# Kernel optimization log

Hardware: AMD Instinct MI355X
Metric: run time of the kernel (lower is better)

The kernel has to match this reference:

```python
import jax, jax.numpy as jnp
import numpy as np

CHANNELS = 32


def _mlp(x, W1, b1, W2, b2, W3, b3):
    # FNN: Linear -> ReLU -> Linear -> ReLU -> Linear (last layer linear)
    h = jax.nn.relu(x @ W1 + b1)
    h = jax.nn.relu(h @ W2 + b2)
    return h @ W3 + b3


def setup_inputs() -> dict:
    key = jax.random.key(0)
    ks = jax.random.split(key, 8)
    E = 262144
    C = CHANNELS
    H = 128
    d_in = 4  # 2 * spatial_dim
    d_out = C * (C + 1)  # 1056
    s = lambda fan_in: 1.0 / np.sqrt(fan_in)
    return {
        "pos_i": jax.random.normal(ks[0], (E, 2), jnp.float32),
        "pos_j": jax.random.normal(ks[1], (E, 2), jnp.float32),
        "v_j": jax.random.normal(ks[2], (E, C), jnp.float32),
        "W1": jax.random.normal(ks[3], (d_in, H), jnp.float32) * s(d_in),
        "b1": jnp.zeros((H,), jnp.float32),
        "W2": jax.random.normal(ks[4], (H, H), jnp.float32) * s(H),
        "b2": jnp.zeros((H,), jnp.float32),
        "W3": jax.random.normal(ks[5], (H, d_out), jnp.float32) * s(H),
        "b3": jnp.zeros((d_out,), jnp.float32),
    }


def reference(pos_i, pos_j, v_j, W1, b1, W2, b2, W3, b3):
    C = CHANNELS
    pos_ij = jnp.concatenate((pos_i, pos_j), axis=-1)          # [E, 2*spatial_dim]
    kernel = _mlp(pos_ij, W1, b1, W2, b2, W3, b3)
    kernel = kernel.reshape(-1, C, C + 1)                      # [E, C, C+1]
    mat, bias = kernel[..., :, :-1], kernel[..., :, -1]        # [E,C,C], [E,C]
    return jnp.einsum('eij,ej->ei', mat, v_j) + bias           # [E, C]
```

## Files before the change

### kernel.cpp

```cpp
#include <hip/hip_runtime.h>


#define E_TOTAL 262144
#define EPB 256
#define NBLK (E_TOTAL / EPB)
#define NEED_WS (524288ull + 67108864ull)

typedef float f32x4 __attribute__((ext_vector_type(4)));
typedef short s8v  __attribute__((ext_vector_type(8)));
typedef unsigned int u32;

__device__ __forceinline__ unsigned short f2bf(float x) {
  unsigned u = __float_as_uint(x);
  u += 0x7fffu + ((u >> 16) & 1u);
  return (unsigned short)(u >> 16);
}

__device__ __forceinline__ void ld16_g2l(const void* g, void* l) {
  __builtin_amdgcn_global_load_lds((const __attribute__((address_space(1))) u32*)g,
                                   (__attribute__((address_space(3))) u32*)l, 16, 0, 0);
}

__global__ void prep_pack(const float* __restrict__ W2, const float* __restrict__ W3,
                          const float* __restrict__ b3,
                          unsigned short* __restrict__ Wg2, unsigned short* __restrict__ W2f,
                          unsigned short* __restrict__ b3f, float* __restrict__ b3c) {
  int idx = blockIdx.x * 256 + threadIdx.x;
  if (idx < 135168) {
    int k = idx / 1056, c = idx % 1056;
    int i = c / 33, jc = c % 33;
    int col = jc * 32 + i;
    int nnt = col >> 4, low = col & 15;
    int nn = (nnt & 1) ? (33 + (nnt >> 1)) : (nnt >> 1);
    int ks = k >> 5, kr = k & 31;
    int lane = ((kr >> 3) << 4) + low;
    int jj = k & 7;
    Wg2[((nn * 4 + ks) * 64 + lane) * 8 + jj] = f2bf(W3[idx]);
  }
  if (idx < 16384) {
    int k = idx >> 7, n = idx & 127;
    int ks = k >> 5, kr = k & 31;
    int nt = n >> 4, low = n & 15;
    int l = ((kr >> 3) << 4) + low;
    int jj = k & 7;
    W2f[((ks * 8 + nt) * 64 + l) * 8 + jj] = f2bf(W2[idx]);
  }
  if (idx < 1024) {
    int jj = idx & 7, lane = (idx >> 3) & 63, ih = idx >> 9;
    int j = ((lane >> 4) << 3) + jj, i = ih * 16 + (lane & 15);
    b3f[idx] = f2bf(b3[i * 33 + j]);
  }
  if (idx < 32) b3c[idx] = b3[idx * 33 + 32];
}

__global__ __launch_bounds__(256, 3) void h2_pass(
    const float* __restrict__ pos_i, const float* __restrict__ pos_j,
    const float* __restrict__ W1, const float* __restrict__ b1,
    const float* __restrict__ b2, const unsigned short* __restrict__ W2f,
    unsigned short* __restrict__ h2frag) {
  __shared__ __attribute__((aligned(16))) char smem[67584];
  unsigned short* h1c = (unsigned short*)smem;
  unsigned short* h2n = (unsigned short*)(smem + 17408);
  unsigned short* W2L = (unsigned short*)(smem + 34816);

  const int tid = threadIdx.x;
  const int w = tid >> 6, lane = tid & 63, q = lane >> 4, ln = lane & 15;
  const int B0 = blockIdx.x * EPB;

  {
    const unsigned short* src = W2f + tid * 8;
    char* dstb = smem + 34816 + w * 1024;
#pragma unroll
    for (int cc = 0; cc < 8; ++cc)
      ld16_g2l(src + cc * 2048, dstb + cc * 4096);
  }

  const int hh0 = (tid & 15) * 8;
  float w1r[4][8], b1r[8], b2r[8];
#pragma unroll
  for (int d = 0; d < 4; ++d)
#pragma unroll
    for (int u = 0; u < 8; ++u) w1r[d][u] = W1[d * 128 + hh0 + u];
#pragma unroll
  for (int u = 0; u < 8; ++u) b1r[u] = b1[hh0 + u];
#pragma unroll
  for (int s = 0; s < 8; ++s) b2r[s] = b2[s * 16 + ln];

  for (int qtr = 0; qtr < 4; ++qtr) {
#pragma unroll
    for (int half = 0; half < 4; ++half) {
      int ee = (tid >> 4) + half * 16;
      int eg = B0 + qtr * 64 + ee;
      float2 pi = *(const float2*)(pos_i + (size_t)eg * 2);
      float2 pj = *(const float2*)(pos_j + (size_t)eg * 2);
      s8v hv;
#pragma unroll
      for (int u = 0; u < 8; ++u) {
        float o = b1r[u] + pi.x * w1r[0][u] + pi.y * w1r[1][u] +
                  pj.x * w1r[2][u] + pj.y * w1r[3][u];
        hv[u] = (short)f2bf(fmaxf(o, 0.f));
      }
      *(s8v*)&h1c[ee * 136 + hh0] = hv;
    }
    __syncthreads();

#pragma unroll
    for (int s = 0; s < 8; ++s) {
      f32x4 a4 = {0.f, 0.f, 0.f, 0.f};
#pragma unroll
      for (int ks = 0; ks < 4; ++ks) {
        s8v afr = *(const s8v*)&h1c[(w * 16 + ln) * 136 + ks * 32 + q * 8];
        s8v bfr = *(const s8v*)&W2L[((ks * 8 + s) * 64 + lane) * 8];
        a4 = __builtin_amdgcn_mfma_f32_16x16x32_bf16(afr, bfr, a4, 0, 0, 0);
      }
      int eb = w * 16 + q * 4;
      int kc = s * 16 + ln;
#pragma unroll
      for (int r = 0; r < 4; ++r)
        h2n[(eb + r) * 136 + kc] = f2bf(fmaxf(a4[r] + b2r[s], 0.f));
    }
    __syncthreads();

    {
      int f = tid >> 4, g = f >> 2, ks = f & 3, s = tid & 15;
      unsigned short* dst =
          h2frag + ((size_t)(blockIdx.x * 16 + qtr * 4 + g) * 4 + ks) * 512;
#pragma unroll
      for (int r4 = 0; r4 < 4; ++r4) {
        int l = s * 4 + r4;
        s8v v = *(const s8v*)&h2n[(g * 16 + (l & 15)) * 136 + ks * 32 + (l >> 4) * 8];
        *(s8v*)&dst[l * 8] = v;
      }
    }
  }
}

__device__ __forceinline__ void tile_load(s8v (&dst)[4], const unsigned short* __restrict__ Wg2,
                                          int n, int lane) {
  const s8v* src = (const s8v*)(Wg2 + (size_t)n * 2048 + lane * 8);
#pragma unroll
  for (int ks = 0; ks < 4; ++ks) dst[ks] = src[ks * 64];
}

__device__ __forceinline__ void tile_compute(const s8v (&bf)[4], const float* __restrict__ vt,
                                             int j, int eoff,
                                             const s8v (&af)[4][4], float (&oa)[4][4]) {
  const f32x4 zero4 = {0.f, 0.f, 0.f, 0.f};
  const float* vp = vt + j * 260 + eoff;
#pragma unroll
  for (int m = 0; m < 4; ++m) {
    f32x4 vv = *(const f32x4*)(vp + m * 16);
    f32x4 p = __builtin_amdgcn_mfma_f32_16x16x32_bf16(af[m][0], bf[0], zero4, 0, 0, 0);
#pragma unroll
    for (int ks = 1; ks < 4; ++ks)
      p = __builtin_amdgcn_mfma_f32_16x16x32_bf16(af[m][ks], bf[ks], p, 0, 0, 0);
#pragma unroll
    for (int r = 0; r < 4; ++r) oa[m][r] += vv[r] * p[r];
  }
}

__device__ __forceinline__ void init_oa(float (&oa)[4][4], const float* __restrict__ vj,
                                        const unsigned short* __restrict__ b3f,
                                        const float* __restrict__ b3c,
                                        int B0, int w, int q, int ln, int lane, int ih) {
  s8v b3fr = *(const s8v*)(b3f + (ih * 64 + lane) * 8);
  float cbv = b3c[ih * 16 + ln];
  f32x4 ci = {cbv, cbv, cbv, cbv};
#pragma unroll
  for (int m = 0; m < 4; ++m) {
    int e = B0 + w * 64 + m * 16 + ln;
    const float4 va = *(const float4*)(vj + (size_t)e * 32 + q * 8);
    const float4 vb = *(const float4*)(vj + (size_t)e * 32 + q * 8 + 4);
    s8v t;
    t[0] = (short)f2bf(va.x); t[1] = (short)f2bf(va.y);
    t[2] = (short)f2bf(va.z); t[3] = (short)f2bf(va.w);
    t[4] = (short)f2bf(vb.x); t[5] = (short)f2bf(vb.y);
    t[6] = (short)f2bf(vb.z); t[7] = (short)f2bf(vb.w);
    f32x4 p = __builtin_amdgcn_mfma_f32_16x16x32_bf16(t, b3fr, ci, 0, 0, 0);
#pragma unroll
    for (int r = 0; r < 4; ++r) oa[m][r] = p[r];
  }
}

__device__ __forceinline__ void store_half(float* __restrict__ out, const float (&oa)[4][4],
                                           int B0, int w, int q, int ln, int ih) {
#pragma unroll
  for (int m = 0; m < 4; ++m)
#pragma unroll
    for (int r = 0; r < 4; ++r) {
      int e = B0 + w * 64 + m * 16 + q * 4 + r;
      out[(size_t)e * 32 + ih * 16 + ln] = oa[m][r];
    }
}

__global__ __launch_bounds__(256, 3) void g_pass(
    const float* __restrict__ vj, const unsigned short* __restrict__ Wg2,
    const unsigned short* __restrict__ b3f, const float* __restrict__ b3c,
    const unsigned short* __restrict__ h2frag, float* __restrict__ out) {
  __shared__ __attribute__((aligned(16))) char smem[34320];
  float* vt = (float*)smem;

  const int tid = threadIdx.x;
  const int w = tid >> 6, lane = tid & 63, q = lane >> 4, ln = lane & 15;
  const int B0 = blockIdx.x * EPB;
  const int eoff = w * 64 + q * 4;

  s8v af[4][4];
#pragma unroll
  for (int m = 0; m < 4; ++m)
#pragma unroll
    for (int ks = 0; ks < 4; ++ks)
      af[m][ks] = *(const s8v*)&h2frag[((size_t)(blockIdx.x * 16 + w * 4 + m) * 4 + ks) * 512 + lane * 8];

  s8v bf[4];
  tile_load(bf, Wg2, 0, lane);

  {
    const float* vrow = vj + (size_t)(B0 + tid) * 32;
#pragma unroll
    for (int j4 = 0; j4 < 8; ++j4) {
      float4 vv = *(const float4*)(vrow + j4 * 4);
      vt[(j4 * 4 + 0) * 260 + tid] = vv.x;
      vt[(j4 * 4 + 1) * 260 + tid] = vv.y;
      vt[(j4 * 4 + 2) * 260 + tid] = vv.z;
      vt[(j4 * 4 + 3) * 260 + tid] = vv.w;
    }
    vt[32 * 260 + tid] = 1.0f;
  }

  float oa[4][4];
  init_oa(oa, vj, b3f, b3c, B0, w, q, ln, lane, 0);

#pragma unroll 1
  for (int n = 0; n < 33; ++n) {
    tile_compute(bf, vt, n, eoff, af, oa);
    tile_load(bf, Wg2, n + 1, lane);
  }

  store_half(out, oa, B0, w, q, ln, 0);
  init_oa(oa, vj, b3f, b3c, B0, w, q, ln, lane, 1);

#pragma unroll 1
  for (int n = 33; n < 66; ++n) {
    tile_compute(bf, vt, n - 33, eoff, af, oa);
    tile_load(bf, Wg2, n + 1, lane);
  }
  store_half(out, oa, B0, w, q, ln, 1);
}

template <int IH>
__device__ __forceinline__ void tile_compute2(const s8v (&bf)[4], const float* __restrict__ vt,
                                              int j, int eoff,
                                              const s8v (&af)[4][4], float (&oa)[2][4][4]) {
  const f32x4 zero4 = {0.f, 0.f, 0.f, 0.f};
  const float* vp = vt + j * 260 + eoff;
#pragma unroll
  for (int m = 0; m < 4; ++m) {
    f32x4 p = __builtin_amdgcn_mfma_f32_16x16x32_bf16(af[m][0], bf[0], zero4, 0, 0, 0);
#pragma unroll
    for (int ks = 1; ks < 4; ++ks)
      p = __builtin_amdgcn_mfma_f32_16x16x32_bf16(af[m][ks], bf[ks], p, 0, 0, 0);
    f32x4 vv = *(const f32x4*)(vp + m * 16);
#pragma unroll
    for (int r = 0; r < 4; ++r) oa[IH][m][r] += vv[r] * p[r];
  }
}

__global__ __launch_bounds__(256, 2) void fnn_fused(
    const float* __restrict__ pos_i, const float* __restrict__ pos_j,
    const float* __restrict__ vj, const float* __restrict__ W1,
    const float* __restrict__ b1, const float* __restrict__ b2,
    const unsigned short* __restrict__ W2f, const unsigned short* __restrict__ Wg2,
    const unsigned short* __restrict__ b3f, const float* __restrict__ b3c,
    float* __restrict__ out) {
  __shared__ __attribute__((aligned(16))) char smem[67584];
  float* vt = (float*)smem;
  unsigned short* h1c = (unsigned short*)smem;
  unsigned short* h2n = (unsigned short*)(smem + 17408);
  unsigned short* W2L = (unsigned short*)(smem + 34816);

  const int tid = threadIdx.x;
  const int w = tid >> 6, lane = tid & 63, q = lane >> 4, ln = lane & 15;
  const int B0 = blockIdx.x * EPB;
  const int eoff = w * 64 + q * 4;

  {
    const unsigned short* src = W2f + tid * 8;
    char* dstb = smem + 34816 + w * 1024;
#pragma unroll
    for (int cc = 0; cc < 8; ++cc)
      ld16_g2l(src + cc * 2048, dstb + cc * 4096);
  }

  float oa[2][4][4];
  {
    s8v av[4];
#pragma unroll
    for (int m = 0; m < 4; ++m) {
      int e = B0 + w * 64 + m * 16 + ln;
      const float4 va = *(const float4*)(vj + (size_t)e * 32 + q * 8);
      const float4 vb = *(const float4*)(vj + (size_t)e * 32 + q * 8 + 4);
      s8v t;
      t[0] = (short)f2bf(va.x); t[1] = (short)f2bf(va.y);
      t[2] = (short)f2bf(va.z); t[3] = (short)f2bf(va.w);
      t[4] = (short)f2bf(vb.x); t[5] = (short)f2bf(vb.y);
      t[6] = (short)f2bf(vb.z); t[7] = (short)f2bf(vb.w);
      av[m] = t;
    }
#pragma unroll
    for (int ih = 0; ih < 2; ++ih) {
      s8v b3fr = *(const s8v*)(b3f + (ih * 64 + lane) * 8);
      float cbv = b3c[ih * 16 + ln];
      f32x4 ci = {cbv, cbv, cbv, cbv};
#pragma unroll
      for (int m = 0; m < 4; ++m) {
        f32x4 p = __builtin_amdgcn_mfma_f32_16x16x32_bf16(av[m], b3fr, ci, 0, 0, 0);
#pragma unroll
        for (int r = 0; r < 4; ++r) oa[ih][m][r] = p[r];
      }
    }
  }

  const int hh0 = (tid & 15) * 8;
  float w1r[4][8], b1r[8], b2r[8];
#pragma unroll
  for (int d = 0; d < 4; ++d)
#pragma unroll
    for (int u = 0; u < 8; ++u) w1r[d][u] = W1[d * 128 + hh0 + u];
#pragma unroll
  for (int u = 0; u < 8; ++u) b1r[u] = b1[hh0 + u];
#pragma unroll
  for (int s = 0; s < 8; ++s) b2r[s] = b2[s * 16 + ln];

  s8v af[4][4];
  for (int qtr = 0; qtr < 4; ++qtr) {
#pragma unroll
    for (int half = 0; half < 4; ++half) {
      int ee = (tid >> 4) + half * 16;
      int eg = B0 + qtr * 64 + ee;
      float2 pi = *(const float2*)(pos_i + (size_t)eg * 2);
      float2 pj = *(const float2*)(pos_j + (size_t)eg * 2);
      s8v hv;
#pragma unroll
      for (int u = 0; u < 8; ++u) {
        float o = b1r[u] + pi.x * w1r[0][u] + pi.y * w1r[1][u] +
                  pj.x * w1r[2][u] + pj.y * w1r[3][u];
        hv[u] = (short)f2bf(fmaxf(o, 0.f));
      }
      *(s8v*)&h1c[ee * 136 + hh0] = hv;
    }
    __syncthreads();
#pragma unroll
    for (int s = 0; s < 8; ++s) {
      f32x4 a4 = {0.f, 0.f, 0.f, 0.f};
#pragma unroll
      for (int ks = 0; ks < 4; ++ks) {
        s8v afr = *(const s8v*)&h1c[(w * 16 + ln) * 136 + ks * 32 + q * 8];
        s8v bfr = *(const s8v*)&W2L[((ks * 8 + s) * 64 + lane) * 8];
        a4 = __builtin_amdgcn_mfma_f32_16x16x32_bf16(afr, bfr, a4, 0, 0, 0);
      }
      int eb = w * 16 + q * 4;
      int kc = s * 16 + ln;
#pragma unroll
      for (int r = 0; r < 4; ++r)
        h2n[(eb + r) * 136 + kc] = f2bf(fmaxf(a4[r] + b2r[s], 0.f));
    }
    __syncthreads();
    if (w == qtr) {
#pragma unroll
      for (int m = 0; m < 4; ++m)
#pragma unroll
        for (int ks = 0; ks < 4; ++ks)
          af[m][ks] = *(const s8v*)&h2n[(m * 16 + ln) * 136 + ks * 32 + q * 8];
    }
    __syncthreads();
  }

  s8v bf[4];
  tile_load(bf, Wg2, 0, lane);

  {
    const float* vrow = vj + (size_t)(B0 + tid) * 32;
#pragma unroll
    for (int j4 = 0; j4 < 8; ++j4) {
      float4 vv = *(const float4*)(vrow + j4 * 4);
      vt[(j4 * 4 + 0) * 260 + tid] = vv.x;
      vt[(j4 * 4 + 1) * 260 + tid] = vv.y;
      vt[(j4 * 4 + 2) * 260 + tid] = vv.z;
      vt[(j4 * 4 + 3) * 260 + tid] = vv.w;
    }
    vt[32 * 260 + tid] = 1.0f;
  }

#pragma unroll 1
  for (int n = 0; n < 33; ++n) {
    tile_compute2<0>(bf, vt, n, eoff, af, oa);
    tile_load(bf, Wg2, n + 1, lane);
  }
#pragma unroll 1
  for (int n = 33; n < 66; ++n) {
    tile_compute2<1>(bf, vt, n - 33, eoff, af, oa);
    tile_load(bf, Wg2, n + 1, lane);
  }

#pragma unroll
  for (int m = 0; m < 4; ++m)
#pragma unroll
    for (int ih = 0; ih < 2; ++ih)
#pragma unroll
      for (int r = 0; r < 4; ++r) {
        int e = B0 + w * 64 + m * 16 + q * 4 + r;
        out[(size_t)e * 32 + ih * 16 + ln] = oa[ih][m][r];
      }
}

extern "C" void kernel_launch(void* const* d_in, const int* in_sizes, int n_in,
                              void* d_out, int out_size, void* d_ws, size_t ws_size,
                              hipStream_t stream) {
  const float* pos_i = (const float*)d_in[0];
  const float* pos_j = (const float*)d_in[1];
  const float* vj    = (const float*)d_in[2];
  const float* W1    = (const float*)d_in[3];
  const float* b1    = (const float*)d_in[4];
  const float* W2    = (const float*)d_in[5];
  const float* b2    = (const float*)d_in[6];
  const float* W3    = (const float*)d_in[7];
  const float* b3    = (const float*)d_in[8];
  float* outp = (float*)d_out;

  unsigned short* Wg2 = (unsigned short*)d_ws;
  unsigned short* W2f = (unsigned short*)((char*)d_ws + 270336);
  unsigned short* b3f = (unsigned short*)((char*)d_ws + 303104);
  float*          b3c = (float*)((char*)d_ws + 305152);
  unsigned short* h2frag = (unsigned short*)((char*)d_ws + 524288);

  prep_pack<<<528, 256, 0, stream>>>(W2, W3, b3, Wg2, W2f, b3f, b3c);
  if (ws_size >= NEED_WS) {
    h2_pass<<<NBLK, 256, 0, stream>>>(pos_i, pos_j, W1, b1, b2, W2f, h2frag);
    g_pass<<<NBLK, 256, 0, stream>>>(vj, Wg2, b3f, b3c, h2frag, outp);
  } else {
    fnn_fused<<<NBLK, 256, 0, stream>>>(pos_i, pos_j, vj, W1, b1, b2, W2f, Wg2, b3f, b3c, outp);
  }
}
```

Baseline: 191.8 us.

## Stage W3 tiles through double-buffered LDS in g_pass; drop W2 LDS staging in h2_pass

In g_pass, the per-tile W3 fragments are no longer loaded from global memory into registers with a one-tile prefetch. They are now streamed two tiles at a time into a double-buffered LDS region with async global-to-LDS loads, with block-wide barriers between chunks. In h2_pass, W2 fragments are read straight from global memory instead of being staged in LDS, which halves its shared memory, and the layer-1 compute now produces 4 columns per thread instead of 8. The intent is to hide W3 load latency and raise h2_pass occupancy, at the cost of extra syncthreads and more LDS in g_pass. Which kernel path the hidden launcher actually calls is unclear.

```diff
diff --git a/kernel.cpp b/kernel.cpp
--- a/kernel.cpp
+++ b/kernel.cpp
@@ -8,6 +8,7 @@
 
 typedef float f32x4 __attribute__((ext_vector_type(4)));
 typedef short s8v  __attribute__((ext_vector_type(8)));
+typedef short s4v  __attribute__((ext_vector_type(4)));
 typedef unsigned int u32;
 
 __device__ __forceinline__ unsigned short f2bf(float x) {
@@ -58,49 +59,40 @@
     const float* __restrict__ W1, const float* __restrict__ b1,
     const float* __restrict__ b2, const unsigned short* __restrict__ W2f,
     unsigned short* __restrict__ h2frag) {
-  __shared__ __attribute__((aligned(16))) char smem[67584];
+  __shared__ __attribute__((aligned(16))) char smem[34816];
   unsigned short* h1c = (unsigned short*)smem;
   unsigned short* h2n = (unsigned short*)(smem + 17408);
-  unsigned short* W2L = (unsigned short*)(smem + 34816);
 
   const int tid = threadIdx.x;
   const int w = tid >> 6, lane = tid & 63, q = lane >> 4, ln = lane & 15;
   const int B0 = blockIdx.x * EPB;
 
-  {
-    const unsigned short* src = W2f + tid * 8;
-    char* dstb = smem + 34816 + w * 1024;
-#pragma unroll
-    for (int cc = 0; cc < 8; ++cc)
-      ld16_g2l(src + cc * 2048, dstb + cc * 4096);
-  }
-
-  const int hh0 = (tid & 15) * 8;
-  float w1r[4][8], b1r[8], b2r[8];
+  const int hh0 = (tid & 31) * 4;
+  float w1r[4][4], b1r4[4], b2r[8];
 #pragma unroll
   for (int d = 0; d < 4; ++d)
 #pragma unroll
-    for (int u = 0; u < 8; ++u) w1r[d][u] = W1[d * 128 + hh0 + u];
-#pragma unroll
-  for (int u = 0; u < 8; ++u) b1r[u] = b1[hh0 + u];
+    for (int u = 0; u < 4; ++u) w1r[d][u] = W1[d * 128 + hh0 + u];
+#pragma unroll
+  for (int u = 0; u < 4; ++u) b1r4[u] = b1[hh0 + u];
 #pragma unroll
   for (int s = 0; s < 8; ++s) b2r[s] = b2[s * 16 + ln];
 
   for (int qtr = 0; qtr < 4; ++qtr) {
 #pragma unroll
-    for (int half = 0; half < 4; ++half) {
-      int ee = (tid >> 4) + half * 16;
+    for (int half = 0; half < 8; ++half) {
+      int ee = (tid >> 5) + half * 8;
       int eg = B0 + qtr * 64 + ee;
       float2 pi = *(const float2*)(pos_i + (size_t)eg * 2);
       float2 pj = *(const float2*)(pos_j + (size_t)eg * 2);
-      s8v hv;
-#pragma unroll
-      for (int u = 0; u < 8; ++u) {
-        float o = b1r[u] + pi.x * w1r[0][u] + pi.y * w1r[1][u] +
+      s4v hv;
+#pragma unroll
+      for (int u = 0; u < 4; ++u) {
+        float o = b1r4[u] + pi.x * w1r[0][u] + pi.y * w1r[1][u] +
                   pj.x * w1r[2][u] + pj.y * w1r[3][u];
         hv[u] = (short)f2bf(fmaxf(o, 0.f));
       }
-      *(s8v*)&h1c[ee * 136 + hh0] = hv;
+      *(s4v*)&h1c[ee * 136 + hh0] = hv;
     }
     __syncthreads();
 
@@ -110,7 +102,7 @@
 #pragma unroll
       for (int ks = 0; ks < 4; ++ks) {
         s8v afr = *(const s8v*)&h1c[(w * 16 + ln) * 136 + ks * 32 + q * 8];
-        s8v bfr = *(const s8v*)&W2L[((ks * 8 + s) * 64 + lane) * 8];
+        s8v bfr = *(const s8v*)(W2f + ((ks * 8 + s) * 64 + lane) * 8);
         a4 = __builtin_amdgcn_mfma_f32_16x16x32_bf16(afr, bfr, a4, 0, 0, 0);
       }
       int eb = w * 16 + q * 4;
@@ -135,25 +127,23 @@
   }
 }
 
-__device__ __forceinline__ void tile_load(s8v (&dst)[4], const unsigned short* __restrict__ Wg2,
-                                          int n, int lane) {
-  const s8v* src = (const s8v*)(Wg2 + (size_t)n * 2048 + lane * 8);
-#pragma unroll
-  for (int ks = 0; ks < 4; ++ks) dst[ks] = src[ks * 64];
-}
-
-__device__ __forceinline__ void tile_compute(const s8v (&bf)[4], const float* __restrict__ vt,
-                                             int j, int eoff,
-                                             const s8v (&af)[4][4], float (&oa)[4][4]) {
+__device__ __forceinline__ void tile_computeL(const unsigned short* __restrict__ buf, int t,
+                                              const float* __restrict__ vt, int j,
+                                              int lane, int eoff,
+                                              const s8v (&af)[4][4], float (&oa)[4][4]) {
   const f32x4 zero4 = {0.f, 0.f, 0.f, 0.f};
+  s8v bfr[4];
+#pragma unroll
+  for (int ks = 0; ks < 4; ++ks)
+    bfr[ks] = *(const s8v*)&buf[(t * 4 + ks) * 512 + lane * 8];
   const float* vp = vt + j * 260 + eoff;
 #pragma unroll
   for (int m = 0; m < 4; ++m) {
     f32x4 vv = *(const f32x4*)(vp + m * 16);
-    f32x4 p = __builtin_amdgcn_mfma_f32_16x16x32_bf16(af[m][0], bf[0], zero4, 0, 0, 0);
+    f32x4 p = __builtin_amdgcn_mfma_f32_16x16x32_bf16(af[m][0], bfr[0], zero4, 0, 0, 0);
 #pragma unroll
     for (int ks = 1; ks < 4; ++ks)
-      p = __builtin_amdgcn_mfma_f32_16x16x32_bf16(af[m][ks], bf[ks], p, 0, 0, 0);
+      p = __builtin_amdgcn_mfma_f32_16x16x32_bf16(af[m][ks], bfr[ks], p, 0, 0, 0);
 #pragma unroll
     for (int r = 0; r < 4; ++r) oa[m][r] += vv[r] * p[r];
   }
@@ -197,23 +187,29 @@
     const float* __restrict__ vj, const unsigned short* __restrict__ Wg2,
     const unsigned short* __restrict__ b3f, const float* __restrict__ b3c,
     const unsigned short* __restrict__ h2frag, float* __restrict__ out) {
-  __shared__ __attribute__((aligned(16))) char smem[34320];
+  __shared__ __attribute__((aligned(16))) char smem[50704];
   float* vt = (float*)smem;
+  unsigned short* Bb  = (unsigned short*)(smem + 34320);
+  char* BbChar = smem + 34320;
 
   const int tid = threadIdx.x;
   const int w = tid >> 6, lane = tid & 63, q = lane >> 4, ln = lane & 15;
   const int B0 = blockIdx.x * EPB;
   const int eoff = w * 64 + q * 4;
 
+  {
+    const unsigned short* src = Wg2 + tid * 8;
+    char* dstb = BbChar + w * 1024;
+    ld16_g2l(src, dstb);
+    ld16_g2l(src + 2048, dstb + 4096);
+  }
+
   s8v af[4][4];
 #pragma unroll
   for (int m = 0; m < 4; ++m)
 #pragma unroll
     for (int ks = 0; ks < 4; ++ks)
       af[m][ks] = *(const s8v*)&h2frag[((size_t)(blockIdx.x * 16 + w * 4 + m) * 4 + ks) * 512 + lane * 8];
-
-  s8v bf[4];
-  tile_load(bf, Wg2, 0, lane);
 
   {
     const float* vrow = vj + (size_t)(B0 + tid) * 32;
@@ -230,22 +226,56 @@
 
   float oa[4][4];
   init_oa(oa, vj, b3f, b3c, B0, w, q, ln, lane, 0);
+  __syncthreads();
 
 #pragma unroll 1
-  for (int n = 0; n < 33; ++n) {
-    tile_compute(bf, vt, n, eoff, af, oa);
-    tile_load(bf, Wg2, n + 1, lane);
-  }
-
-  store_half(out, oa, B0, w, q, ln, 0);
-  init_oa(oa, vj, b3f, b3c, B0, w, q, ln, lane, 1);
-
+  for (int c = 0; c < 16; ++c) {
+    const unsigned short* buf = Bb + (c & 1) * 4096;
+    {
+      const unsigned short* src = Wg2 + (size_t)(c + 1) * 4096 + tid * 8;
+      char* dstb = BbChar + ((c + 1) & 1) * 8192 + w * 1024;
+      ld16_g2l(src, dstb);
+      ld16_g2l(src + 2048, dstb + 4096);
+    }
+    tile_computeL(buf, 0, vt, 2 * c,     lane, eoff, af, oa);
+    tile_computeL(buf, 1, vt, 2 * c + 1, lane, eoff, af, oa);
+    __syncthreads();
+  }
+  {
+    const unsigned short* buf = Bb;
+    {
+      const unsigned short* src = Wg2 + (size_t)17 * 4096 + tid * 8;
+      char* dstb = BbChar + 8192 + w * 1024;
+      ld16_g2l(src, dstb);
+      ld16_g2l(src + 2048, dstb + 4096);
+    }
+    tile_computeL(buf, 0, vt, 32, lane, eoff, af, oa);
+    store_half(out, oa, B0, w, q, ln, 0);
+    init_oa(oa, vj, b3f, b3c, B0, w, q, ln, lane, 1);
+    tile_computeL(buf, 1, vt, 0, lane, eoff, af, oa);
+    __syncthreads();
+  }
 #pragma unroll 1
-  for (int n = 33; n < 66; ++n) {
-    tile_compute(bf, vt, n - 33, eoff, af, oa);
-    tile_load(bf, Wg2, n + 1, lane);
+  for (int c = 17; c < 33; ++c) {
+    const unsigned short* buf = Bb + (c & 1) * 4096;
+    if (c < 32) {
+      const unsigned short* src = Wg2 + (size_t)(c + 1) * 4096 + tid * 8;
+      char* dstb = BbChar + ((c + 1) & 1) * 8192 + w * 1024;
+      ld16_g2l(src, dstb);
+      ld16_g2l(src + 2048, dstb + 4096);
+    }
+    tile_computeL(buf, 0, vt, 2 * c - 33, lane, eoff, af, oa);
+    tile_computeL(buf, 1, vt, 2 * c - 32, lane, eoff, af, oa);
+    __syncthreads();
   }
   store_half(out, oa, B0, w, q, ln, 1);
+}
+
+__device__ __forceinline__ void tile_load(s8v (&dst)[4], const unsigned short* __restrict__ Wg2,
+                                          int n, int lane) {
+  const s8v* src = (const s8v*)(Wg2 + (size_t)n * 2048 + lane * 8);
+#pragma unroll
+  for (int ks = 0; ks < 4; ++ks) dst[ks] = src[ks * 64];
 }
 
 template <int IH>
```

After: 230.8 us. +20.4%, slower.
